# Performance work log

Measured on AMD Instinct MI355X. Metric: run time of the kernel, lower is better.

Reference implementation:

```python
import jax, jax.numpy as jnp
import numpy as np

# --- static module config (from init_kwargs) ---
C1_OUT = 64          # c1OutChannels
C1K = 400            # k winners in conv layer
N_FC = 1024          # fc1 hidden units (n)
K_FC = 100           # k winners in fc1
BOOST = 1.0          # boostStrength
W_SPARSITY = 0.5     # weightSparsity: fraction of fc1 weights allowed nonzero
HP = 12              # pooled spatial size: floor((28-5+1)/2)
C1_OUTPUT_LEN = C1_OUT * HP * HP  # 9216
BATCH = 4096


def setup_inputs() -> dict:
    key = jax.random.key(0)
    ks = jax.random.split(key, 10)
    x = jax.random.normal(ks[0], (BATCH, 1, 28, 28), jnp.float32)
    c1_w = jax.random.normal(ks[1], (C1_OUT, 1, 5, 5), jnp.float32) * 0.1
    c1_b = jax.random.normal(ks[2], (C1_OUT,), jnp.float32) * 0.01
    # duty cycles live in [0, ~density]
    duty_cnn = jax.random.uniform(ks[3], (1, C1_OUT, 1, 1), jnp.float32) * 0.05
    fc1_w = jax.random.normal(ks[4], (N_FC, C1_OUT_LEN_ := C1_OUTPUT_LEN), jnp.float32) * 0.01
    fc1_mask_raw = jax.random.uniform(ks[5], (N_FC, C1_OUTPUT_LEN), jnp.float32)
    fc1_b = jax.random.normal(ks[6], (N_FC,), jnp.float32) * 0.01
    duty_fc = jax.random.uniform(ks[7], (N_FC,), jnp.float32) * 0.1
    fc2_w = jax.random.normal(ks[8], (10, N_FC), jnp.float32) * 0.05
    fc2_b = jnp.zeros((10,), jnp.float32)
    return dict(x=x, c1_w=c1_w, c1_b=c1_b, duty_cnn=duty_cnn, fc1_w=fc1_w,
                fc1_mask_raw=fc1_mask_raw, fc1_b=fc1_b, duty_fc=duty_fc,
                fc2_w=fc2_w, fc2_b=fc2_b)


def _kwinners(x_flat, boost_flat, k):
    """Duty-cycle-boosted k-winner mask.
    x_flat: [B, N]; boost_flat: [1, N] broadcastable boost factors.
    Keeps original x values at the top-k boosted positions per row, zeros rest.
    Boosting uses stop_gradient(x), matching KWinners*.forward(x.detach()*boost).
    """
    boosted = jax.lax.stop_gradient(x_flat) * boost_flat
    thr = jax.lax.top_k(boosted, k)[0][:, -1:]  # k-th largest per row
    return jnp.where(boosted >= thr, x_flat, jnp.zeros((), x_flat.dtype))


def reference(x, c1_w, c1_b, duty_cnn, fc1_w, fc1_mask_raw, fc1_b, duty_fc,
              fc2_w, fc2_b):
    B = x.shape[0]
    # conv2d (valid, stride 1) -> [B, 64, 24, 24]
    y = jax.lax.conv_general_dilated(
        x, c1_w, window_strides=(1, 1), padding='VALID',
        dimension_numbers=('NCHW', 'OIHW', 'NCHW')) + c1_b[None, :, None, None]
    # max_pool2d(2) -> [B, 64, 12, 12]
    y = jax.lax.reduce_window(y, -jnp.inf, jax.lax.max,
                              (1, 1, 2, 2), (1, 1, 2, 2), 'VALID')
    # KWinnersCNN: global top-k over flattened (C,H,W), per-channel boost
    target_density = C1K / C1_OUTPUT_LEN
    boost_c = jnp.exp((target_density - duty_cnn) * BOOST)  # [1,C,1,1]
    boost_flat = jnp.broadcast_to(boost_c, (1, C1_OUT, HP, HP)).reshape(1, -1)
    yf = _kwinners(y.reshape(B, -1), boost_flat, C1K)  # [B, 9216]
    # LinearSDR fc1: sparse-weight linear + KWinners
    w_mask = (fc1_mask_raw < W_SPARSITY).astype(fc1_w.dtype)
    h = yf @ (fc1_w * w_mask).T + fc1_b  # [B, 1024]
    boost_fc = jnp.exp((K_FC / N_FC - duty_fc) * BOOST)[None, :]
    h = _kwinners(h, boost_fc, K_FC)
    # fc2 + log_softmax (dropout inactive in eval mode)
    logits = h @ fc2_w.T + fc2_b
    return jax.nn.log_softmax(logits, axis=1)
```

## Files before the change

kernel.cpp:

```cpp
#include <hip/hip_runtime.h>

__device__ __forceinline__ float b2f(unsigned short u) {
  return __uint_as_float(((unsigned)u) << 16);
}
__device__ __forceinline__ unsigned short f2b(float f) {
  unsigned u = __float_as_uint(f);
  return (unsigned short)((u + 0x7FFFu + ((u >> 16) & 1u)) >> 16);
}
__device__ __forceinline__ float gload(const void* p, int i, int isb) {
  return isb ? b2f(((const unsigned short*)p)[i]) : ((const float*)p)[i];
}
__device__ __forceinline__ unsigned tokey(float f) {
  unsigned u = __float_as_uint(f);
  return u ^ (unsigned)(((int)u >> 31) | 0x80000000u);
}

__global__ void k_detect(const void* x, int* flag) {
  int tid = threadIdx.x;
  unsigned short u = ((const unsigned short*)x)[2 * tid];
  int e = (u >> 7) & 0xFF;
  bool sane = (e >= 100 && e <= 140);
  unsigned long long m = __ballot(sane);
  if (tid == 0) *flag = (__popcll(m) >= 40) ? 1 : 0;
}

__global__ __launch_bounds__(256) void k_prep(const void* __restrict__ fc1w,
                                              const void* __restrict__ mraw,
                                              float* __restrict__ WtF,
                                              const int* __restrict__ flag) {
  __shared__ float tile[64][65];
  const int isb = *flag;
  const int i0 = blockIdx.x * 64;
  const int u0 = blockIdx.y * 64;
  const int tx = threadIdx.x & 63, ty = threadIdx.x >> 6;
  for (int uu = ty; uu < 64; uu += 4) {
    int gi = (u0 + uu) * 9216 + i0 + tx;
    float wv = gload(fc1w, gi, isb);
    float mv = gload(mraw, gi, isb);
    tile[uu][tx] = (mv < 0.5f) ? wv : 0.0f;
  }
  __syncthreads();
  for (int ii = ty; ii < 64; ii += 4)
    WtF[(i0 + ii) * 1024 + u0 + tx] = tile[tx][ii];
}

__global__ __launch_bounds__(256) void k_conv(const void* __restrict__ x,
                                              const void* __restrict__ c1w_g,
                                              const void* __restrict__ c1b_g,
                                              const void* __restrict__ duty_g,
                                              int2* __restrict__ wpair,
                                              int* __restrict__ wcnt,
                                              const int* __restrict__ flag) {
  __shared__ __align__(16) unsigned char u_imghist[3136];
  __shared__ float cb[64], bcs[64];
  __shared__ __align__(16) float pooled[9216];
  __shared__ unsigned wtot[4];
  __shared__ unsigned selb, selk;
  float* img = (float*)u_imghist;
  unsigned* h2a = (unsigned*)u_imghist;
  unsigned* h2b = (unsigned*)(u_imghist + 1024);
  const int tid = threadIdx.x;
  const int b = blockIdx.x;
  const int isb = *flag;
  const int lane = tid & 63;
  const int wv_id = tid >> 6;

  for (int i = tid; i < 784; i += 256) img[i] = gload(x, b * 784 + i, isb);
  if (tid < 64) {
    cb[tid] = gload(c1b_g, tid, isb);
    float arg = (float)(400.0 / 9216.0) - gload(duty_g, tid, isb);
    bcs[tid] = (float)exp((double)arg);
  }
  __syncthreads();

  {
    const int c = tid >> 2;
    const int half = tid & 1;
    const int ph0 = ((tid >> 1) & 1) * 6;
    float w[25];
#pragma unroll
    for (int i = 0; i < 25; ++i) w[i] = gload(c1w_g, c * 25 + i, isb);
    const float bias = cb[c];
    float R[6][16];
#pragma unroll
    for (int r = 0; r < 6; ++r) {
      int ir = 2 * ph0 + r;
#pragma unroll
      for (int q = 0; q < 4; ++q)
        ((float4*)&R[r][0])[q] = ((const float4*)img)[ir * 7 + half * 3 + q];
    }
#pragma unroll
    for (int i = 0; i < 6; ++i) {
      const int ph = ph0 + i;
      float a0[12], a1[12];
#pragma unroll
      for (int j = 0; j < 12; ++j) { a0[j] = 0.f; a1[j] = 0.f; }
#pragma unroll
      for (int kj = 0; kj < 5; ++kj) {
#pragma unroll
        for (int kr = 0; kr < 5; ++kr) {
          float wk = w[kr * 5 + kj];
          const float* r0 = &R[(2 * i + kr) % 6][0];
          const float* r1 = &R[(2 * i + kr + 1) % 6][0];
#pragma unroll
          for (int j = 0; j < 12; ++j) {
            a0[j] = fmaf(r0[j + kj], wk, a0[j]);
            a1[j] = fmaf(r1[j + kj], wk, a1[j]);
          }
        }
      }
      int obase = c * 144 + ph * 12 + half * 6;
#pragma unroll
      for (int q = 0; q < 6; ++q) {
        float m = fmaxf(fmaxf(a0[2 * q], a0[2 * q + 1]),
                        fmaxf(a1[2 * q], a1[2 * q + 1]));
        pooled[obase + q] = m + bias;
      }
      if (i < 5) {
        int ir0 = 2 * ph + 6, ir1 = 2 * ph + 7;
        float* d0 = &R[(2 * i) % 6][0];
        float* d1 = &R[(2 * i + 1) % 6][0];
#pragma unroll
        for (int q = 0; q < 4; ++q) {
          ((float4*)d0)[q] = ((const float4*)img)[ir0 * 7 + half * 3 + q];
          ((float4*)d1)[q] = ((const float4*)img)[ir1 * 7 + half * 3 + q];
        }
      }
    }
  }
  __syncthreads();

  unsigned keys[36];
  {
    const float bcf = bcs[tid >> 2];
#pragma unroll
    for (int e4 = 0; e4 < 9; ++e4) {
      float4 pv = ((float4*)pooled)[tid * 9 + e4];
      keys[4 * e4 + 0] = tokey(pv.x * bcf);
      keys[4 * e4 + 1] = tokey(pv.y * bcf);
      keys[4 * e4 + 2] = tokey(pv.z * bcf);
      keys[4 * e4 + 3] = tokey(pv.w * bcf);
    }
  }

  unsigned kfix = 0;
  unsigned kk = 400;
  for (int pass = 3; pass >= 0; --pass) {
    const int shift = pass * 8;
    const unsigned himask = (pass == 3) ? 0u : (0xFFFFFFFFu << (shift + 8));
    h2a[tid] = 0;
    h2b[tid] = 0;
    __syncthreads();
    unsigned* myh = (wv_id < 2) ? h2a : h2b;
    if (pass == 3) {
      unsigned cbin = keys[0] >> 24, ccnt = 1;
#pragma unroll
      for (int e = 1; e < 36; ++e) {
        unsigned bin = keys[e] >> 24;
        if (bin == cbin) {
          ++ccnt;
        } else {
          atomicAdd(&myh[cbin], ccnt);
          cbin = bin;
          ccnt = 1;
        }
      }
      atomicAdd(&myh[cbin], ccnt);
    } else {
#pragma unroll
      for (int e = 0; e < 36; ++e) {
        unsigned key = keys[e];
        if (((key ^ kfix) & himask) == 0)
          atomicAdd(&myh[(key >> shift) & 255u], 1u);
      }
    }
    __syncthreads();
    unsigned own = h2a[tid] + h2b[tid];
    unsigned v = own;
#pragma unroll
    for (int off = 1; off < 64; off <<= 1) {
      unsigned y = __shfl_down(v, off, 64);
      if (lane + off < 64) v += y;
    }
    if (lane == 0) wtot[wv_id] = v;
    __syncthreads();
#pragma unroll
    for (int w2 = 0; w2 < 4; ++w2)
      if (w2 > wv_id) v += wtot[w2];
    unsigned snext = v - own;
    if (v >= kk && snext < kk) {
      selb = (unsigned)tid;
      selk = kk - snext;
    }
    __syncthreads();
    kfix |= selb << shift;
    kk = selk;
  }

  unsigned mycnt = 0;
#pragma unroll
  for (int e = 0; e < 36; ++e) mycnt += (keys[e] >= kfix) ? 1u : 0u;
  unsigned px = mycnt;
#pragma unroll
  for (int off = 1; off < 64; off <<= 1) {
    unsigned y = __shfl_up(px, off, 64);
    if (lane >= off) px += y;
  }
  if (lane == 63) wtot[wv_id] = px;
  __syncthreads();
  unsigned base = 0;
#pragma unroll
  for (int w2 = 0; w2 < 4; ++w2)
    if (w2 < wv_id) base += wtot[w2];
  int pos = (int)(base + px - mycnt);
  for (int e = 0; e < 36; ++e) {
    if (keys[e] >= kfix) {
      int o = tid * 36 + e;
      if (pos < 512)
        wpair[b * 512 + pos] = make_int2(__float_as_int(pooled[o]), o << 12);
      ++pos;
    }
  }
  if (tid == 0) {
    unsigned tot = wtot[0] + wtot[1] + wtot[2] + wtot[3];
    wcnt[b] = (int)(tot < 512u ? tot : 512u);
  }
}

__global__ __launch_bounds__(128) void k_fc1(const float* __restrict__ WtF,
                                             const int2* __restrict__ wpair,
                                             const int* __restrict__ wcnt,
                                             const void* __restrict__ fc1b,
                                             float* __restrict__ h,
                                             const int* __restrict__ flag,
                                             int img_base) {
  __shared__ __align__(16) int2 wl[512];
  const int tid = threadIdx.x;
  const int img = img_base + (blockIdx.x >> 3);
  const int slice = blockIdx.x & 7;
  const int isb = *flag;
  const int cnt = wcnt[img];
  const int2* __restrict__ wp = wpair + img * 512;
  for (int i = tid; i < cnt; i += 128) wl[i] = wp[i];
  __syncthreads();
  const int u = (slice << 7) + tid;
  const char* __restrict__ Wb = (const char*)WtF + (unsigned)u * 4u;
  const int4* wl4 = (const int4*)wl;
  float acc = 0.f;
  int w = 0;
  for (; w + 8 <= cnt; w += 8) {
    const int b4 = w >> 1;
    int4 q0 = wl4[b4 + 0];
    int4 q1 = wl4[b4 + 1];
    int4 q2 = wl4[b4 + 2];
    int4 q3 = wl4[b4 + 3];
    acc = fmaf(__int_as_float(q0.x), *(const float*)(Wb + (unsigned)q0.y), acc);
    acc = fmaf(__int_as_float(q0.z), *(const float*)(Wb + (unsigned)q0.w), acc);
    acc = fmaf(__int_as_float(q1.x), *(const float*)(Wb + (unsigned)q1.y), acc);
    acc = fmaf(__int_as_float(q1.z), *(const float*)(Wb + (unsigned)q1.w), acc);
    acc = fmaf(__int_as_float(q2.x), *(const float*)(Wb + (unsigned)q2.y), acc);
    acc = fmaf(__int_as_float(q2.z), *(const float*)(Wb + (unsigned)q2.w), acc);
    acc = fmaf(__int_as_float(q3.x), *(const float*)(Wb + (unsigned)q3.y), acc);
    acc = fmaf(__int_as_float(q3.z), *(const float*)(Wb + (unsigned)q3.w), acc);
  }
  for (; w < cnt; ++w) {
    int2 p = wl[w];
    acc = fmaf(__int_as_float(p.x), *(const float*)(Wb + (unsigned)p.y), acc);
  }
  h[img * 1024 + u] = acc + gload(fc1b, u, isb);
}

__global__ __launch_bounds__(256) void k_boost(const void* __restrict__ dutyfc,
                                               float* __restrict__ bf,
                                               const int* __restrict__ flag) {
  const int u = blockIdx.x * 256 + threadIdx.x;
  const int isb = *flag;
  if (u < 1024)
    bf[u] = (float)exp((double)(0.09765625f - gload(dutyfc, u, isb)));
}

__global__ __launch_bounds__(256) void k_sel(const float* __restrict__ h,
                                             const float* __restrict__ bf,
                                             const void* __restrict__ fc2w,
                                             const void* __restrict__ fc2b,
                                             void* __restrict__ out,
                                             const int* __restrict__ flag) {
  __shared__ unsigned hist4[4][256];
  __shared__ unsigned wtot[4];
  __shared__ unsigned selb, selk;
  __shared__ double lg[10];
  __shared__ double mred[2];
  const int tid = threadIdx.x;
  const int row = blockIdx.x;
  const int isb = *flag;
  const int lane = tid & 63;
  const int wv_id = tid >> 6;
  if (tid < 10) lg[tid] = (double)gload(fc2b, tid, isb);
  __syncthreads();

  const int u0 = 2 * tid, u1 = 2 * tid + 1, u2 = 512 + 2 * tid, u3 = 513 + 2 * tid;
  float2 hlo = ((const float2*)(h + row * 1024))[tid];
  float2 hhi = ((const float2*)(h + row * 1024 + 512))[tid];
  float h0 = hlo.x, h1 = hlo.y, h2 = hhi.x, h3 = hhi.y;
  float2 blo = ((const float2*)bf)[tid];
  float2 bhi = ((const float2*)(bf + 512))[tid];
  unsigned k0 = tokey(h0 * blo.x);
  unsigned k1 = tokey(h1 * blo.y);
  unsigned k2 = tokey(h2 * bhi.x);
  unsigned k3 = tokey(h3 * bhi.y);

  unsigned kfix = 0;
  unsigned kk = 100;
  for (int pass = 3; pass >= 0; --pass) {
    const int shift = pass * 8;
    const unsigned himask = (pass == 3) ? 0u : (0xFFFFFFFFu << (shift + 8));
#pragma unroll
    for (int w2 = 0; w2 < 4; ++w2) hist4[w2][tid] = 0;
    __syncthreads();
    unsigned* myh = hist4[wv_id];
    if (((k0 ^ kfix) & himask) == 0) atomicAdd(&myh[(k0 >> shift) & 255u], 1u);
    if (((k1 ^ kfix) & himask) == 0) atomicAdd(&myh[(k1 >> shift) & 255u], 1u);
    if (((k2 ^ kfix) & himask) == 0) atomicAdd(&myh[(k2 >> shift) & 255u], 1u);
    if (((k3 ^ kfix) & himask) == 0) atomicAdd(&myh[(k3 >> shift) & 255u], 1u);
    __syncthreads();
    unsigned own = hist4[0][tid] + hist4[1][tid] + hist4[2][tid] + hist4[3][tid];
    unsigned v = own;
#pragma unroll
    for (int off = 1; off < 64; off <<= 1) {
      unsigned y = __shfl_down(v, off, 64);
      if (lane + off < 64) v += y;
    }
    if (lane == 0) wtot[wv_id] = v;
    __syncthreads();
#pragma unroll
    for (int w2 = 0; w2 < 4; ++w2)
      if (w2 > wv_id) v += wtot[w2];
    unsigned snext = v - own;
    if (v >= kk && snext < kk) {
      selb = (unsigned)tid;
      selk = kk - snext;
    }
    __syncthreads();
    kfix |= selb << shift;
    kk = selk;
  }
  bool kp0 = k0 >= kfix, kp1 = k1 >= kfix, kp2 = k2 >= kfix, kp3 = k3 >= kfix;

  double part[10];
#pragma unroll
  for (int c = 0; c < 10; ++c) part[c] = 0.0;
  if (kp0) {
#pragma unroll
    for (int c = 0; c < 10; ++c) part[c] = fma((double)h0, (double)gload(fc2w, c * 1024 + u0, isb), part[c]);
  }
  if (kp1) {
#pragma unroll
    for (int c = 0; c < 10; ++c) part[c] = fma((double)h1, (double)gload(fc2w, c * 1024 + u1, isb), part[c]);
  }
  if (kp2) {
#pragma unroll
    for (int c = 0; c < 10; ++c) part[c] = fma((double)h2, (double)gload(fc2w, c * 1024 + u2, isb), part[c]);
  }
  if (kp3) {
#pragma unroll
    for (int c = 0; c < 10; ++c) part[c] = fma((double)h3, (double)gload(fc2w, c * 1024 + u3, isb), part[c]);
  }
#pragma unroll
  for (int c = 0; c < 10; ++c) {
    double p = part[c];
    for (int off = 32; off > 0; off >>= 1) p += __shfl_xor(p, off);
    if ((tid & 63) == 0) atomicAdd(&lg[c], p);
  }
  __syncthreads();
  if (tid == 0) {
    double m = lg[0];
#pragma unroll
    for (int c = 1; c < 10; ++c) m = lg[c] > m ? lg[c] : m;
    double sum = 0.0;
#pragma unroll
    for (int c = 0; c < 10; ++c) sum += exp(lg[c] - m);
    mred[0] = m;
    mred[1] = log(sum);
  }
  __syncthreads();
  if (tid < 10) {
    double o = lg[tid] - mred[0] - mred[1];
    if (isb)
      ((unsigned short*)out)[row * 10 + tid] = f2b((float)o);
    else
      ((float*)out)[row * 10 + tid] = (float)o;
  }
}

extern "C" void kernel_launch(void* const* d_in, const int* in_sizes, int n_in,
                              void* d_out, int out_size, void* d_ws, size_t ws_size,
                              hipStream_t stream) {
  char* ws = (char*)d_ws;
  float* WtF = (float*)ws;
  int2* wpair = (int2*)(ws + 37748736);
  int* wcnt = (int*)(ws + 54525952);
  float* h = (float*)(ws + 54542336);
  int* flag = (int*)(ws + 71319552);
  float* bf = WtF;

  k_detect<<<1, 64, 0, stream>>>(d_in[0], flag);
  k_prep<<<dim3(144, 16), 256, 0, stream>>>(d_in[4], d_in[5], WtF, flag);
  k_conv<<<4096, 256, 0, stream>>>(d_in[0], d_in[1], d_in[2], d_in[3],
                                   wpair, wcnt, flag);
  k_fc1<<<2048 * 8, 128, 0, stream>>>(WtF, wpair, wcnt, d_in[6], h, flag, 0);
  k_fc1<<<2048 * 8, 128, 0, stream>>>(WtF, wpair, wcnt, d_in[6], h, flag, 2048);
  k_boost<<<4, 256, 0, stream>>>(d_in[7], bf, flag);
  k_sel<<<4096, 256, 0, stream>>>(h, bf, d_in[8], d_in[9], d_out, flag);
}
```

Baseline: 584.1 us.

## Process one row per wavefront in k-winner selection and merge fc1 launches

The fc1/top-k selection kernel now assigns one row to each 64-lane wavefront instead of one row per 256-thread block. The radix histogram, prefix scan, bucket selection, fc2 reduction and log-softmax then run with wave-local shared memory, ballots and shuffles, with no block-wide barriers. The two half-batch fc1 launches are also merged into one launch over all images. Each lane now holds 16 values in registers, which raises register pressure, and all same-wave atomics land on a single histogram.

```diff
diff --git a/kernel.cpp b/kernel.cpp
--- a/kernel.cpp
+++ b/kernel.cpp
@@ -232,11 +232,10 @@
                                              const int* __restrict__ wcnt,
                                              const void* __restrict__ fc1b,
                                              float* __restrict__ h,
-                                             const int* __restrict__ flag,
-                                             int img_base) {
+                                             const int* __restrict__ flag) {
   __shared__ __align__(16) int2 wl[512];
   const int tid = threadIdx.x;
-  const int img = img_base + (blockIdx.x >> 3);
+  const int img = blockIdx.x >> 3;
   const int slice = blockIdx.x & 7;
   const int isb = *flag;
   const int cnt = wcnt[img];
@@ -285,110 +284,107 @@
                                              const void* __restrict__ fc2b,
                                              void* __restrict__ out,
                                              const int* __restrict__ flag) {
-  __shared__ unsigned hist4[4][256];
-  __shared__ unsigned wtot[4];
-  __shared__ unsigned selb, selk;
-  __shared__ double lg[10];
-  __shared__ double mred[2];
+  __shared__ __align__(16) unsigned whist[4][256];
   const int tid = threadIdx.x;
-  const int row = blockIdx.x;
+  const int lane = tid & 63;
+  const int wv = tid >> 6;
+  const int row = blockIdx.x * 4 + wv;
   const int isb = *flag;
-  const int lane = tid & 63;
-  const int wv_id = tid >> 6;
-  if (tid < 10) lg[tid] = (double)gload(fc2b, tid, isb);
-  __syncthreads();
-
-  const int u0 = 2 * tid, u1 = 2 * tid + 1, u2 = 512 + 2 * tid, u3 = 513 + 2 * tid;
-  float2 hlo = ((const float2*)(h + row * 1024))[tid];
-  float2 hhi = ((const float2*)(h + row * 1024 + 512))[tid];
-  float h0 = hlo.x, h1 = hlo.y, h2 = hhi.x, h3 = hhi.y;
-  float2 blo = ((const float2*)bf)[tid];
-  float2 bhi = ((const float2*)(bf + 512))[tid];
-  unsigned k0 = tokey(h0 * blo.x);
-  unsigned k1 = tokey(h1 * blo.y);
-  unsigned k2 = tokey(h2 * bhi.x);
-  unsigned k3 = tokey(h3 * bhi.y);
-
-  unsigned kfix = 0;
-  unsigned kk = 100;
+  unsigned* hist = whist[wv];
+  volatile unsigned* vhist = whist[wv];
+
+  float hv[16];
+  unsigned keys[16];
+#pragma unroll
+  for (int j = 0; j < 16; ++j) {
+    float xv = h[row * 1024 + j * 64 + lane];
+    hv[j] = xv;
+    keys[j] = tokey(xv * bf[j * 64 + lane]);
+  }
+
+  unsigned kfix = 0, kk = 100;
   for (int pass = 3; pass >= 0; --pass) {
     const int shift = pass * 8;
     const unsigned himask = (pass == 3) ? 0u : (0xFFFFFFFFu << (shift + 8));
-#pragma unroll
-    for (int w2 = 0; w2 < 4; ++w2) hist4[w2][tid] = 0;
-    __syncthreads();
-    unsigned* myh = hist4[wv_id];
-    if (((k0 ^ kfix) & himask) == 0) atomicAdd(&myh[(k0 >> shift) & 255u], 1u);
-    if (((k1 ^ kfix) & himask) == 0) atomicAdd(&myh[(k1 >> shift) & 255u], 1u);
-    if (((k2 ^ kfix) & himask) == 0) atomicAdd(&myh[(k2 >> shift) & 255u], 1u);
-    if (((k3 ^ kfix) & himask) == 0) atomicAdd(&myh[(k3 >> shift) & 255u], 1u);
-    __syncthreads();
-    unsigned own = hist4[0][tid] + hist4[1][tid] + hist4[2][tid] + hist4[3][tid];
-    unsigned v = own;
+    ((uint4*)hist)[lane] = make_uint4(0u, 0u, 0u, 0u);
+    __builtin_amdgcn_sched_barrier(0);
+#pragma unroll
+    for (int j = 0; j < 16; ++j) {
+      if (((keys[j] ^ kfix) & himask) == 0)
+        atomicAdd(&hist[(keys[j] >> shift) & 255u], 1u);
+    }
+    __builtin_amdgcn_sched_barrier(0);
+    unsigned o0 = vhist[4 * lane + 0];
+    unsigned o1 = vhist[4 * lane + 1];
+    unsigned o2 = vhist[4 * lane + 2];
+    unsigned o3 = vhist[4 * lane + 3];
+    unsigned lsum = o0 + o1 + o2 + o3;
+    unsigned v = lsum;
 #pragma unroll
     for (int off = 1; off < 64; off <<= 1) {
       unsigned y = __shfl_down(v, off, 64);
       if (lane + off < 64) v += y;
     }
-    if (lane == 0) wtot[wv_id] = v;
-    __syncthreads();
-#pragma unroll
-    for (int w2 = 0; w2 < 4; ++w2)
-      if (w2 > wv_id) v += wtot[w2];
-    unsigned snext = v - own;
-    if (v >= kk && snext < kk) {
-      selb = (unsigned)tid;
-      selk = kk - snext;
-    }
-    __syncthreads();
-    kfix |= selb << shift;
-    kk = selk;
-  }
-  bool kp0 = k0 >= kfix, kp1 = k1 >= kfix, kp2 = k2 >= kfix, kp3 = k3 >= kfix;
+    const unsigned after = v - lsum;
+    const unsigned t3 = o3;
+    const unsigned t2 = o2 + t3;
+    const unsigned t1 = o1 + t2;
+    const unsigned t0 = o0 + t1;
+    unsigned candb = 0, candk = 0;
+    bool found = false;
+    const unsigned S0 = after + t0, S1 = after + t1, S2 = after + t2,
+                   S3 = after + t3, S4 = after;
+    if (S0 >= kk && S1 < kk) { candb = 4u * lane + 0u; candk = kk - S1; found = true; }
+    else if (S1 >= kk && S2 < kk) { candb = 4u * lane + 1u; candk = kk - S2; found = true; }
+    else if (S2 >= kk && S3 < kk) { candb = 4u * lane + 2u; candk = kk - S3; found = true; }
+    else if (S3 >= kk && S4 < kk) { candb = 4u * lane + 3u; candk = kk - S4; found = true; }
+    unsigned long long msk = __ballot(found);
+    int src = __ffsll((unsigned long long)msk) - 1;
+    candb = __shfl(candb, src, 64);
+    candk = __shfl(candk, src, 64);
+    kfix |= candb << shift;
+    kk = candk;
+  }
 
   double part[10];
 #pragma unroll
   for (int c = 0; c < 10; ++c) part[c] = 0.0;
-  if (kp0) {
-#pragma unroll
-    for (int c = 0; c < 10; ++c) part[c] = fma((double)h0, (double)gload(fc2w, c * 1024 + u0, isb), part[c]);
-  }
-  if (kp1) {
-#pragma unroll
-    for (int c = 0; c < 10; ++c) part[c] = fma((double)h1, (double)gload(fc2w, c * 1024 + u1, isb), part[c]);
-  }
-  if (kp2) {
-#pragma unroll
-    for (int c = 0; c < 10; ++c) part[c] = fma((double)h2, (double)gload(fc2w, c * 1024 + u2, isb), part[c]);
-  }
-  if (kp3) {
-#pragma unroll
-    for (int c = 0; c < 10; ++c) part[c] = fma((double)h3, (double)gload(fc2w, c * 1024 + u3, isb), part[c]);
+#pragma unroll
+  for (int j = 0; j < 16; ++j) {
+    if (keys[j] >= kfix) {
+      const int u = j * 64 + lane;
+      const double hx = (double)hv[j];
+#pragma unroll
+      for (int c = 0; c < 10; ++c)
+        part[c] = fma(hx, (double)gload(fc2w, c * 1024 + u, isb), part[c]);
+    }
   }
 #pragma unroll
   for (int c = 0; c < 10; ++c) {
     double p = part[c];
+#pragma unroll
     for (int off = 32; off > 0; off >>= 1) p += __shfl_xor(p, off);
-    if ((tid & 63) == 0) atomicAdd(&lg[c], p);
-  }
-  __syncthreads();
-  if (tid == 0) {
-    double m = lg[0];
-#pragma unroll
-    for (int c = 1; c < 10; ++c) m = lg[c] > m ? lg[c] : m;
-    double sum = 0.0;
-#pragma unroll
-    for (int c = 0; c < 10; ++c) sum += exp(lg[c] - m);
-    mred[0] = m;
-    mred[1] = log(sum);
-  }
-  __syncthreads();
-  if (tid < 10) {
-    double o = lg[tid] - mred[0] - mred[1];
+    part[c] = p + (double)gload(fc2b, c, isb);
+  }
+
+  double m = part[0];
+#pragma unroll
+  for (int c = 1; c < 10; ++c) m = part[c] > m ? part[c] : m;
+  double mv = part[0];
+#pragma unroll
+  for (int c = 1; c < 10; ++c)
+    if (lane == c) mv = part[c];
+  double e = (lane < 10) ? exp(mv - m) : 0.0;
+  double sum = 0.0;
+#pragma unroll
+  for (int c = 0; c < 10; ++c) sum += __shfl(e, c, 64);
+  double logs = log(sum);
+  if (lane < 10) {
+    double o = mv - m - logs;
     if (isb)
-      ((unsigned short*)out)[row * 10 + tid] = f2b((float)o);
+      ((unsigned short*)out)[row * 10 + lane] = f2b((float)o);
     else
-      ((float*)out)[row * 10 + tid] = (float)o;
+      ((float*)out)[row * 10 + lane] = (float)o;
   }
 }
 
@@ -407,8 +403,7 @@
   k_prep<<<dim3(144, 16), 256, 0, stream>>>(d_in[4], d_in[5], WtF, flag);
   k_conv<<<4096, 256, 0, stream>>>(d_in[0], d_in[1], d_in[2], d_in[3],
                                    wpair, wcnt, flag);
-  k_fc1<<<2048 * 8, 128, 0, stream>>>(WtF, wpair, wcnt, d_in[6], h, flag, 0);
-  k_fc1<<<2048 * 8, 128, 0, stream>>>(WtF, wpair, wcnt, d_in[6], h, flag, 2048);
+  k_fc1<<<4096 * 8, 128, 0, stream>>>(WtF, wpair, wcnt, d_in[6], h, flag);
   k_boost<<<4, 256, 0, stream>>>(d_in[7], bf, flag);
-  k_sel<<<4096, 256, 0, stream>>>(h, bf, d_in[8], d_in[9], d_out, flag);
-}
+  k_sel<<<1024, 256, 0, stream>>>(h, bf, d_in[8], d_in[9], d_out, flag);
+}
```

Result: faster. 564.7 us (-3.3%).
